# Kernel tuning notes

Hardware: AMD Instinct MI355X
Metric: run time of the kernel (lower is better)

The kernel has to match this reference:

```python
import jax, jax.numpy as jnp
import numpy as np

NV, NJ, NB_POSE = 778, 16, 135
PARENTS = np.array([-1, 0, 1, 2, 0, 4, 5, 0, 7, 8, 0, 10, 11, 0, 13, 14], dtype=np.int32)
FINGER_IDX = np.array([734, 333, 443, 555, 678], dtype=np.int32)


def setup_inputs() -> dict:
    key = jax.random.key(0)
    ks = jax.random.split(key, 9)
    B = 4096
    return {
        "beta": jax.random.normal(ks[0], (B, 10), jnp.float32) * 0.3,
        "theta": jax.random.normal(ks[1], (B, 48), jnp.float32) * 0.3,
        "v_template": jax.random.normal(ks[2], (NV, 3), jnp.float32) * 0.05,
        "shapedirs": jax.random.normal(ks[3], (10, NV * 3), jnp.float32) * 0.01,
        "posedirs": jax.random.normal(ks[4], (NB_POSE, NV * 3), jnp.float32) * 0.01,
        "J_regressor": jax.random.uniform(ks[5], (NV, NJ), jnp.float32) / NV,
        "weights": jax.random.uniform(ks[6], (NV, NJ), jnp.float32),
        "hands_mean": jax.random.normal(ks[7], (45,), jnp.float32) * 0.1,
        "hands_components": jax.random.normal(ks[8], (45, 45), jnp.float32) * 0.1,
    }


def batch_rodrigues(r):
    """Axis-angle [N,3] -> rotation matrices [N,3,3] (Rodrigues formula)."""
    eps = 1e-8
    angle = jnp.linalg.norm(r + eps, axis=1, keepdims=True)          # [N,1]
    axis = r / angle
    x, y, z = axis[:, 0], axis[:, 1], axis[:, 2]
    zeros = jnp.zeros_like(x)
    K = jnp.stack([zeros, -z, y, z, zeros, -x, -y, x, zeros], axis=1).reshape(-1, 3, 3)
    a = angle[:, :, None]                                            # [N,1,1]
    I3 = jnp.eye(3, dtype=r.dtype)
    return I3 + jnp.sin(a) * K + (1.0 - jnp.cos(a)) * (K @ K)


def global_rigid_transform(Rs, Js):
    """Rs [B,16,3,3], Js [B,16,3] -> relative skinning transforms A [B,16,4,4]."""
    B = Rs.shape[0]
    bot = jnp.broadcast_to(jnp.array([0.0, 0.0, 0.0, 1.0], Rs.dtype), (B, 1, 4))

    def make_A(R, t):  # R [B,3,3], t [B,3] -> [B,4,4]
        return jnp.concatenate([jnp.concatenate([R, t[:, :, None]], axis=2), bot], axis=1)

    results = [make_A(Rs[:, 0], Js[:, 0])]
    for i in range(1, NJ):  # fixed small kinematic chain
        t = Js[:, i] - Js[:, PARENTS[i]]
        results.append(results[PARENTS[i]] @ make_A(Rs[:, i], t))
    res = jnp.stack(results, axis=1)                                 # [B,16,4,4]
    Js_h = jnp.concatenate([Js, jnp.zeros((B, NJ, 1), Rs.dtype)], axis=2)  # [B,16,4]
    init_bone = jnp.einsum('bjpq,bjq->bjp', res, Js_h)               # [B,16,4]
    return res.at[:, :, :, 3].add(-init_bone)                        # A = res - pack(res @ [J;0])


def reference(beta, theta, v_template, shapedirs, posedirs, J_regressor, weights,
              hands_mean, hands_components):
    B = beta.shape[0]
    P = theta.shape[1] - 3
    # full pose: global rot + PCA-recovered local rotations
    full_local = theta[:, 3:] @ hands_components[:P, :] + hands_mean  # [B,45]
    pose = jnp.concatenate([theta[:, :3], full_local], axis=1)       # [B,48]

    # shape blend
    v_shaped = (beta @ shapedirs).reshape(B, NV, 3) + v_template     # [B,778,3]
    J = jnp.einsum('bvc,vj->bjc', v_shaped, J_regressor)             # [B,16,3]

    # pose blend
    Rs = batch_rodrigues(pose.reshape(-1, 3)).reshape(B, NJ, 3, 3)
    pose_feature = (Rs[:, 1:] - jnp.eye(3, dtype=Rs.dtype)).reshape(B, NB_POSE)
    v_posed = (pose_feature @ posedirs).reshape(B, NV, 3) + v_shaped

    # kinematic chain + linear blend skinning
    A = global_rigid_transform(Rs, J)                                # [B,16,4,4]
    T = jnp.einsum('vj,bjpq->bvpq', weights, A)                      # [B,778,4,4]
    v_homo = jnp.concatenate([v_posed, jnp.ones((B, NV, 1), v_posed.dtype)], axis=2)
    verts = jnp.einsum('bvpq,bvq->bvp', T, v_homo)[:, :, :3]         # [B,778,3]

    joints = jnp.einsum('bvc,vj->bjc', verts, J_regressor)           # [B,16,3]
    joints = jnp.concatenate([joints, verts[:, FINGER_IDX, :]], axis=1)  # [B,21,3]
    return joints
```

## Files before the change

### kernel.cpp

```cpp
#include <hip/hip_runtime.h>

#define NV  778
#define NBP 135
#define NK  146
#define NKQ 152
#define GC  8
#define VCH 98

#define FV0 734
#define FV1 333
#define FV2 443
#define FV3 555
#define FV4 678

__device__ __forceinline__ const float* d_row(int k,
                                              const float* vt,
                                              const float* sd,
                                              const float* pd) {
    return (k == 0) ? vt : (k <= 10 ? sd + (size_t)(k-1)*(NV*3)
                                    : pd + (size_t)(k-11)*(NV*3));
}

__launch_bounds__(256)
__global__ void k_fold(const float* __restrict__ vt,
                       const float* __restrict__ sd,
                       const float* __restrict__ pd,
                       const float* __restrict__ jreg,
                       const float* __restrict__ wts,
                       float* __restrict__ SJ, float* __restrict__ JT,
                       float* __restrict__ WJ, float* __restrict__ Gq,
                       float* __restrict__ Dfing, float* __restrict__ Wfing)
{
    const int o = blockIdx.x;
    const int tid = threadIdx.x;

    if (o < 1168) {
        const int k = o >> 3, chunk = o & 7;
        const int J = tid >> 4, j = tid & 15;
        const float* Drow = d_row(k, vt, sd, pd);
        const int v0 = chunk * VCH;
        const int v1 = (v0 + VCH < NV) ? (v0 + VCH) : NV;
        float a0 = 0.f, a1 = 0.f, a2 = 0.f;
        #pragma unroll 4
        for (int v = v0; v < v1; ++v) {
            float pv = jreg[v*16 + J] * wts[v*16 + j];
            a0 += Drow[3*v+0] * pv;
            a1 += Drow[3*v+1] * pv;
            a2 += Drow[3*v+2] * pv;
        }
        float* gp = Gq + ((size_t)k*256 + tid)*3;
        atomicAdd(gp+0, a0);
        atomicAdd(gp+1, a1);
        atomicAdd(gp+2, a2);
    } else if (o < 1300) {
        const int idx = (o - 1168)*4 + (tid >> 6);
        const int t = tid & 63;
        const float* src; int jc;
        if (idx < 480) { int k = idx / 48; jc = idx % 48; src = sd + (size_t)k*(NV*3); }
        else           { jc = idx - 480;              src = vt; }
        int j = jc / 3, c = jc % 3;
        float acc = 0.f;
        for (int v = t; v < NV; v += 64)
            acc += src[3*v + c] * jreg[v*16 + j];
        for (int off = 32; off; off >>= 1) acc += __shfl_down(acc, off, 64);
        if (t == 0) { if (idx < 480) SJ[idx] = acc; else JT[jc] = acc; }
    } else if (o < 1364) {
        const int cidx = (o - 1300)*4 + (tid >> 6);
        const int t = tid & 63;
        const int J = cidx >> 4, j = cidx & 15;
        float acc = 0.f;
        for (int v = t; v < NV; v += 64)
            acc += jreg[v*16 + J] * wts[v*16 + j];
        for (int off = 32; off; off >>= 1) acc += __shfl_down(acc, off, 64);
        if (t == 0) WJ[cidx] = acc;
    } else {
        const int fv[5] = {FV0, FV1, FV2, FV3, FV4};
        for (int e = tid; e < NK*15; e += 256) {
            int k = e / 15, r = e % 15, f = r / 3, q = r % 3;
            Dfing[e] = d_row(k, vt, sd, pd)[3*fv[f] + q];
        }
        if (tid < 80) {
            int f = tid >> 4, j = tid & 15;
            Wfing[tid] = wts[fv[f]*16 + j];
        }
    }
}

__launch_bounds__(256)
__global__ void kC(const float* __restrict__ beta,
                   const float* __restrict__ theta,
                   const float* __restrict__ hm,
                   const float* __restrict__ hc,
                   const float* __restrict__ SJ,
                   const float* __restrict__ JT,
                   const float* __restrict__ WJ,
                   const float* __restrict__ Gq,
                   const float* __restrict__ Dfing,
                   const float* __restrict__ Wfing,
                   float* __restrict__ out,
                   int Btot)
{
    const int tid = threadIdx.x;
    const int w = tid >> 6, t = tid & 63;
    const int b0 = blockIdx.x * GC;

    __shared__ float s_SJ[480];
    __shared__ float s_JT[48];
    __shared__ float s_WJ[256];
    __shared__ float s_beta[GC][10];
    __shared__ __align__(16) float s_coef[GC][152];
    __shared__ float s_A[GC][192];
    __shared__ float s_vpf[GC][16];
    __shared__ __align__(16) char s_un[GC*768*4];
    float* s_S    = (float*)s_un;
    float* u_hc   = (float*)s_un;
    float* u_th   = u_hc + 2025;
    float* u_pose = u_th + GC*48;
    float* u_J    = u_pose + GC*48;
    float* u_R    = u_J + GC*48;

    for (int i = tid; i < 2025; i += 256) u_hc[i] = hc[i];
    for (int i = tid; i < 480;  i += 256) s_SJ[i] = SJ[i];
    if (tid < 48) s_JT[tid] = JT[tid];
    s_WJ[tid] = WJ[tid];
    for (int i = tid; i < GC*48; i += 256) {
        int g = i / 48, tt = i % 48, b = b0 + g;
        u_th[g*48 + tt] = (b < Btot) ? theta[(size_t)b*48 + tt] : 0.f;
    }
    for (int i = tid; i < GC*10; i += 256) {
        int g = i / 10, k = i % 10, b = b0 + g;
        s_beta[g][k] = (b < Btot) ? beta[(size_t)b*10 + k] : 0.f;
    }
    for (int i = tid; i < GC*152; i += 256) ((float*)s_coef)[i] = 0.f;
    __syncthreads();

    #pragma unroll
    for (int pp = 0; pp < 2; ++pp) {
        int g = pp*4 + w;
        int b = b0 + g;
        if (b < Btot) {
            float* pose = u_pose + g*48;
            float* Jg   = u_J + g*48;
            float* Rg   = u_R + g*144;
            const float* th = u_th + g*48;
            if (t < 3) pose[t] = th[t];
            if (t < 45) {
                float acc = hm[t];
                #pragma unroll 9
                for (int k = 0; k < 45; ++k) acc += th[3+k] * u_hc[k*45 + t];
                pose[3+t] = acc;
            }
            if (t < 48) {
                float acc = s_JT[t];
                #pragma unroll
                for (int k = 0; k < 10; ++k) acc += s_beta[g][k] * s_SJ[k*48 + t];
                Jg[t] = acc;
            }
            if (t < 10) s_coef[g][1+t] = s_beta[g][t];
            if (t == 10) s_coef[g][0] = 1.f;
            if (t < 16) {
                float rx = pose[3*t], ry = pose[3*t+1], rz = pose[3*t+2];
                float ex = rx + 1e-8f, ey = ry + 1e-8f, ez = rz + 1e-8f;
                float angle = sqrtf(ex*ex + ey*ey + ez*ez);
                float inv = 1.f / angle;
                float x = rx*inv, y = ry*inv, z = rz*inv;
                float s  = sinf(angle);
                float c1 = 1.f - cosf(angle);
                float R[9];
                R[0] = 1.f + c1*(-(z*z + y*y));
                R[1] = -s*z + c1*(x*y);
                R[2] =  s*y + c1*(x*z);
                R[3] =  s*z + c1*(x*y);
                R[4] = 1.f + c1*(-(x*x + z*z));
                R[5] = -s*x + c1*(y*z);
                R[6] = -s*y + c1*(x*z);
                R[7] =  s*x + c1*(y*z);
                R[8] = 1.f + c1*(-(x*x + y*y));
                #pragma unroll
                for (int i = 0; i < 9; ++i) Rg[t*9 + i] = R[i];
                if (t >= 1) {
                    #pragma unroll
                    for (int i = 0; i < 9; ++i)
                        s_coef[g][11 + (t-1)*9 + i] = R[i] - ((i % 4 == 0) ? 1.f : 0.f);
                }
            }
            if (t < 16) {
                float res[12];
                #pragma unroll
                for (int p = 0; p < 3; ++p) {
                    res[p*4+0] = Rg[p*3+0];
                    res[p*4+1] = Rg[p*3+1];
                    res[p*4+2] = Rg[p*3+2];
                    res[p*4+3] = Jg[p];
                }
                if (t >= 1) {
                    int start = ((t-1)/3)*3 + 1;
                    int d = t - start;
                    for (int s = 0; s < 3; ++s) {
                        if (s <= d) {
                            int a  = start + s;
                            int pa = (s == 0) ? 0 : (a - 1);
                            float ax = Jg[a*3+0] - Jg[pa*3+0];
                            float ay = Jg[a*3+1] - Jg[pa*3+1];
                            float az = Jg[a*3+2] - Jg[pa*3+2];
                            float nr[12];
                            #pragma unroll
                            for (int p = 0; p < 3; ++p) {
                                float r0 = res[p*4+0], r1 = res[p*4+1], r2 = res[p*4+2];
                                #pragma unroll
                                for (int q = 0; q < 3; ++q)
                                    nr[p*4+q] = r0*Rg[a*9+q] + r1*Rg[a*9+3+q] + r2*Rg[a*9+6+q];
                                nr[p*4+3] = r0*ax + r1*ay + r2*az + res[p*4+3];
                            }
                            #pragma unroll
                            for (int q = 0; q < 12; ++q) res[q] = nr[q];
                        }
                    }
                }
                float jx = Jg[t*3+0], jy = Jg[t*3+1], jz = Jg[t*3+2];
                #pragma unroll
                for (int p = 0; p < 3; ++p) {
                    float r0 = res[p*4+0], r1 = res[p*4+1], r2 = res[p*4+2];
                    float ib = r0*jx + r1*jy + r2*jz;
                    s_A[g][t*12 + p*4+0] = r0;
                    s_A[g][t*12 + p*4+1] = r1;
                    s_A[g][t*12 + p*4+2] = r2;
                    s_A[g][t*12 + p*4+3] = res[p*4+3] - ib;
                }
            }
        }
    }
    __syncthreads();

    {
        float acc[GC][3];
        #pragma unroll
        for (int g = 0; g < GC; ++g) { acc[g][0]=0.f; acc[g][1]=0.f; acc[g][2]=0.f; }
        for (int k = 0; k < NKQ; k += 8) {
            float g0[8], g1[8], g2[8];
            #pragma unroll
            for (int kk = 0; kk < 8; ++kk) {
                const float* gq = Gq + ((size_t)(k+kk)*256 + tid)*3;
                g0[kk] = gq[0]; g1[kk] = gq[1]; g2[kk] = gq[2];
            }
            #pragma unroll
            for (int g = 0; g < GC; ++g) {
                float4 cA = *(const float4*)&s_coef[g][k];
                float4 cB = *(const float4*)&s_coef[g][k+4];
                float cf[8] = {cA.x,cA.y,cA.z,cA.w, cB.x,cB.y,cB.z,cB.w};
                #pragma unroll
                for (int kk = 0; kk < 8; ++kk) {
                    acc[g][0] += cf[kk]*g0[kk];
                    acc[g][1] += cf[kk]*g1[kk];
                    acc[g][2] += cf[kk]*g2[kk];
                }
            }
        }
        __syncthreads();
        #pragma unroll
        for (int g = 0; g < GC; ++g) {
            s_S[g*768 + tid*3 + 0] = acc[g][0];
            s_S[g*768 + tid*3 + 1] = acc[g][1];
            s_S[g*768 + tid*3 + 2] = acc[g][2];
        }
    }
    __syncthreads();

    for (int o = tid; o < GC*48; o += 256) {
        int g = o / 48, rem = o % 48, J = rem / 3, p = rem % 3;
        int b = b0 + g;
        if (b < Btot) {
            const float* Ag = s_A[g];
            const float* Sg = s_S + g*768 + J*48;
            float val = 0.f;
            #pragma unroll
            for (int j = 0; j < 16; ++j) {
                val += Ag[j*12 + p*4 + 0] * Sg[j*3+0]
                     + Ag[j*12 + p*4 + 1] * Sg[j*3+1]
                     + Ag[j*12 + p*4 + 2] * Sg[j*3+2]
                     + Ag[j*12 + p*4 + 3] * s_WJ[J*16 + j];
            }
            out[(size_t)b*63 + J*3 + p] = val;
        }
    }

    if (tid < GC*15) {
        int g = tid / 15, r = tid % 15;
        float acc = 0.f;
        #pragma unroll 4
        for (int k = 0; k < NK; ++k) acc += s_coef[g][k] * Dfing[k*15 + r];
        s_vpf[g][r] = acc;
    }
    __syncthreads();
    if (tid < GC*15) {
        int g = tid / 15, r = tid % 15, f = r / 3, p = r % 3;
        int b = b0 + g;
        if (b < Btot) {
            const float* Ag = s_A[g];
            float vx = s_vpf[g][f*3+0], vy = s_vpf[g][f*3+1], vz = s_vpf[g][f*3+2];
            float val = 0.f;
            #pragma unroll
            for (int j = 0; j < 16; ++j) {
                float wj = Wfing[f*16 + j];
                val += wj * (Ag[j*12 + p*4 + 0]*vx +
                             Ag[j*12 + p*4 + 1]*vy +
                             Ag[j*12 + p*4 + 2]*vz +
                             Ag[j*12 + p*4 + 3]);
            }
            out[(size_t)b*63 + (16+f)*3 + p] = val;
        }
    }
}

extern "C" void kernel_launch(void* const* d_in, const int* in_sizes, int n_in,
                              void* d_out, int out_size, void* d_ws, size_t ws_size,
                              hipStream_t stream) {
    const float* beta       = (const float*)d_in[0];
    const float* theta      = (const float*)d_in[1];
    const float* v_template = (const float*)d_in[2];
    const float* shapedirs  = (const float*)d_in[3];
    const float* posedirs   = (const float*)d_in[4];
    const float* J_reg      = (const float*)d_in[5];
    const float* weights    = (const float*)d_in[6];
    const float* hands_mean = (const float*)d_in[7];
    const float* hands_comp = (const float*)d_in[8];
    float* out = (float*)d_out;

    const int B = in_sizes[0] / 10;

    float* W = (float*)d_ws;
    float* SJ    = W;
    float* JT    = W + 480;
    float* WJ    = W + 528;
    float* Dfing = W + 784;
    float* Wfing = W + 2974;
    float* Gq    = W + 3072;

    hipMemsetAsync(Gq, 0, (size_t)NKQ*768*sizeof(float), stream);
    k_fold<<<1365, 256, 0, stream>>>(v_template, shapedirs, posedirs, J_reg, weights,
                                     SJ, JT, WJ, Gq, Dfing, Wfing);
    kC<<<(B + GC - 1)/GC, 256, 0, stream>>>(beta, theta, hands_mean, hands_comp,
                                            SJ, JT, WJ, Gq, Dfing, Wfing, out, B);
}
```

Measured before the change: 140.5 us.

## Halve batch per block, split fold work finer, and prefetch Gq in registers

Each main-kernel block now processes 4 samples instead of 8, one per wavefront, which doubles the block count and drops the two-pass per-sample loop. The fold kernel splits vertices into 16 chunks instead of 8, giving more blocks and more atomics. The Gq contraction loop becomes software-pipelined: it prefetches the next 8 rows into registers while computing the current ones, and the first batch is issued before shared-memory setup. The finger and joint output stages are moved onto disjoint thread ranges so they can run concurrently. In exchange, each block re-reads the full Gq table for half as many samples, and register pressure rises.

```diff
diff --git a/kernel.cpp b/kernel.cpp
--- a/kernel.cpp
+++ b/kernel.cpp
@@ -4,8 +4,8 @@
 #define NBP 135
 #define NK  146
 #define NKQ 152
-#define GC  8
-#define VCH 98
+#define GC  4
+#define VCH 49
 
 #define FV0 734
 #define FV1 333
@@ -34,14 +34,14 @@
     const int o = blockIdx.x;
     const int tid = threadIdx.x;
 
-    if (o < 1168) {
-        const int k = o >> 3, chunk = o & 7;
+    if (o < 2336) {
+        const int k = o >> 4, chunk = o & 15;
         const int J = tid >> 4, j = tid & 15;
         const float* Drow = d_row(k, vt, sd, pd);
         const int v0 = chunk * VCH;
         const int v1 = (v0 + VCH < NV) ? (v0 + VCH) : NV;
         float a0 = 0.f, a1 = 0.f, a2 = 0.f;
-        #pragma unroll 4
+        #pragma unroll 7
         for (int v = v0; v < v1; ++v) {
             float pv = jreg[v*16 + J] * wts[v*16 + j];
             a0 += Drow[3*v+0] * pv;
@@ -52,8 +52,8 @@
         atomicAdd(gp+0, a0);
         atomicAdd(gp+1, a1);
         atomicAdd(gp+2, a2);
-    } else if (o < 1300) {
-        const int idx = (o - 1168)*4 + (tid >> 6);
+    } else if (o < 2468) {
+        const int idx = (o - 2336)*4 + (tid >> 6);
         const int t = tid & 63;
         const float* src; int jc;
         if (idx < 480) { int k = idx / 48; jc = idx % 48; src = sd + (size_t)k*(NV*3); }
@@ -64,8 +64,8 @@
             acc += src[3*v + c] * jreg[v*16 + j];
         for (int off = 32; off; off >>= 1) acc += __shfl_down(acc, off, 64);
         if (t == 0) { if (idx < 480) SJ[idx] = acc; else JT[jc] = acc; }
-    } else if (o < 1364) {
-        const int cidx = (o - 1300)*4 + (tid >> 6);
+    } else if (o < 2532) {
+        const int cidx = (o - 2468)*4 + (tid >> 6);
         const int t = tid & 63;
         const int J = cidx >> 4, j = cidx & 15;
         float acc = 0.f;
@@ -111,13 +111,20 @@
     __shared__ __align__(16) float s_coef[GC][152];
     __shared__ float s_A[GC][192];
     __shared__ float s_vpf[GC][16];
-    __shared__ __align__(16) char s_un[GC*768*4];
+    __shared__ __align__(16) char s_un[3177*4];
     float* s_S    = (float*)s_un;
     float* u_hc   = (float*)s_un;
     float* u_th   = u_hc + 2025;
     float* u_pose = u_th + GC*48;
     float* u_J    = u_pose + GC*48;
     float* u_R    = u_J + GC*48;
+
+    float cur0[8], cur1[8], cur2[8];
+    #pragma unroll
+    for (int kk = 0; kk < 8; ++kk) {
+        const float* gq = Gq + ((size_t)kk*256 + tid)*3;
+        cur0[kk] = gq[0]; cur1[kk] = gq[1]; cur2[kk] = gq[2];
+    }
 
     for (int i = tid; i < 2025; i += 256) u_hc[i] = hc[i];
     for (int i = tid; i < 480;  i += 256) s_SJ[i] = SJ[i];
@@ -134,10 +141,9 @@
     for (int i = tid; i < GC*152; i += 256) ((float*)s_coef)[i] = 0.f;
     __syncthreads();
 
-    #pragma unroll
-    for (int pp = 0; pp < 2; ++pp) {
-        int g = pp*4 + w;
-        int b = b0 + g;
+    {
+        const int g = w;
+        const int b = b0 + g;
         if (b < Btot) {
             float* pose = u_pose + g*48;
             float* Jg   = u_J + g*48;
@@ -237,11 +243,13 @@
         #pragma unroll
         for (int g = 0; g < GC; ++g) { acc[g][0]=0.f; acc[g][1]=0.f; acc[g][2]=0.f; }
         for (int k = 0; k < NKQ; k += 8) {
-            float g0[8], g1[8], g2[8];
-            #pragma unroll
-            for (int kk = 0; kk < 8; ++kk) {
-                const float* gq = Gq + ((size_t)(k+kk)*256 + tid)*3;
-                g0[kk] = gq[0]; g1[kk] = gq[1]; g2[kk] = gq[2];
+            float nxt0[8], nxt1[8], nxt2[8];
+            if (k + 8 < NKQ) {
+                #pragma unroll
+                for (int kk = 0; kk < 8; ++kk) {
+                    const float* gq = Gq + ((size_t)(k+8+kk)*256 + tid)*3;
+                    nxt0[kk] = gq[0]; nxt1[kk] = gq[1]; nxt2[kk] = gq[2];
+                }
             }
             #pragma unroll
             for (int g = 0; g < GC; ++g) {
@@ -250,9 +258,15 @@
                 float cf[8] = {cA.x,cA.y,cA.z,cA.w, cB.x,cB.y,cB.z,cB.w};
                 #pragma unroll
                 for (int kk = 0; kk < 8; ++kk) {
-                    acc[g][0] += cf[kk]*g0[kk];
-                    acc[g][1] += cf[kk]*g1[kk];
-                    acc[g][2] += cf[kk]*g2[kk];
+                    acc[g][0] += cf[kk]*cur0[kk];
+                    acc[g][1] += cf[kk]*cur1[kk];
+                    acc[g][2] += cf[kk]*cur2[kk];
+                }
+            }
+            if (k + 8 < NKQ) {
+                #pragma unroll
+                for (int kk = 0; kk < 8; ++kk) {
+                    cur0[kk] = nxt0[kk]; cur1[kk] = nxt1[kk]; cur2[kk] = nxt2[kk];
                 }
             }
         }
@@ -266,8 +280,8 @@
     }
     __syncthreads();
 
-    for (int o = tid; o < GC*48; o += 256) {
-        int g = o / 48, rem = o % 48, J = rem / 3, p = rem % 3;
+    if (tid < GC*48) {
+        int g = tid / 48, rem = tid % 48, J = rem / 3, p = rem % 3;
         int b = b0 + g;
         if (b < Btot) {
             const float* Ag = s_A[g];
@@ -284,16 +298,18 @@
         }
     }
 
-    if (tid < GC*15) {
-        int g = tid / 15, r = tid % 15;
+    if (tid >= 192 && tid < 192 + GC*15) {
+        int r2 = tid - 192;
+        int g = r2 / 15, r = r2 % 15;
         float acc = 0.f;
         #pragma unroll 4
         for (int k = 0; k < NK; ++k) acc += s_coef[g][k] * Dfing[k*15 + r];
         s_vpf[g][r] = acc;
     }
     __syncthreads();
-    if (tid < GC*15) {
-        int g = tid / 15, r = tid % 15, f = r / 3, p = r % 3;
+    if (tid >= 192 && tid < 192 + GC*15) {
+        int r2 = tid - 192;
+        int g = r2 / 15, r = r2 % 15, f = r / 3, p = r % 3;
         int b = b0 + g;
         if (b < Btot) {
             const float* Ag = s_A[g];
@@ -337,7 +353,7 @@
     float* Gq    = W + 3072;
 
     hipMemsetAsync(Gq, 0, (size_t)NKQ*768*sizeof(float), stream);
-    k_fold<<<1365, 256, 0, stream>>>(v_template, shapedirs, posedirs, J_reg, weights,
+    k_fold<<<2533, 256, 0, stream>>>(v_template, shapedirs, posedirs, J_reg, weights,
                                      SJ, JT, WJ, Gq, Dfing, Wfing);
     kC<<<(B + GC - 1)/GC, 256, 0, stream>>>(beta, theta, hands_mean, hands_comp,
                                             SJ, JT, WJ, Gq, Dfing, Wfing, out, B);
```

New measurement: 137.8 us. About the same (-1.9%).
